# Kernel optimization log

Measured on AMD Instinct MI355X. Metric: run time of the kernel, lower is better.

## Reference

```python
import jax, jax.numpy as jnp
import numpy as np

EMBED = 1024

def setup_inputs() -> dict:
    key = jax.random.key(0)
    ks = jax.random.split(key, 7)
    s = 1.0 / np.sqrt(EMBED)
    x = jax.random.normal(ks[0], (8, 2048, EMBED), dtype=jnp.float32)
    Wq = jax.random.normal(ks[1], (EMBED, EMBED), dtype=jnp.float32) * s
    bq = jax.random.normal(ks[2], (EMBED,), dtype=jnp.float32) * s
    Wk = jax.random.normal(ks[3], (EMBED, EMBED), dtype=jnp.float32) * s
    bk = jax.random.normal(ks[4], (EMBED,), dtype=jnp.float32) * s
    Wv = jax.random.normal(ks[5], (EMBED, EMBED), dtype=jnp.float32) * s
    bv = jax.random.normal(ks[6], (EMBED,), dtype=jnp.float32) * s
    return {"x": x, "Wq": Wq, "bq": bq, "Wk": Wk, "bk": bk, "Wv": Wv, "bv": bv}

def reference(x, Wq, bq, Wk, bk, Wv, bv):
    # Linear layers: y = x @ W^T + b (torch convention)
    Q = jnp.einsum('bse,fe->bsf', x, Wq) + bq
    K = jnp.einsum('bse,fe->bsf', x, Wk) + bk
    V = jnp.einsum('bse,fe->bsf', x, Wv) + bv
    scale = 1.0 / jnp.sqrt(jnp.asarray(x.shape[-1], x.dtype))
    scores = jnp.einsum('bqe,bke->bqk', Q, K) * scale  # [B, S, S]
    weights = jax.nn.softmax(scores, axis=-1)
    # dropout is identity in eval mode (deterministic reference)
    return jnp.einsum('bqk,bke->bqe', weights, V)
```

## Files before the change

kernel.cpp:

```cpp
#include <hip/hip_runtime.h>

typedef __bf16 bf16x8 __attribute__((ext_vector_type(8)));
typedef float f32x4 __attribute__((ext_vector_type(4)));
typedef _Float16 f16x8v __attribute__((ext_vector_type(8)));
typedef unsigned short u16x8 __attribute__((ext_vector_type(8)));

__device__ __forceinline__ unsigned short f2bf(float f) {
  unsigned int u = __builtin_bit_cast(unsigned int, f);
  u += 0x7fffu + ((u >> 16) & 1u);
  return (unsigned short)(u >> 16);
}

__device__ __forceinline__ unsigned short f2h(float f) {
  _Float16 h = (_Float16)f;
  return __builtin_bit_cast(unsigned short, h);
}

__device__ __forceinline__ void async16(const void* g, void* l) {
  __builtin_amdgcn_global_load_lds(
      (const __attribute__((address_space(1))) unsigned int*)g,
      (__attribute__((address_space(3))) unsigned int*)l, 16, 0, 0);
}

#define MFMA(a, b, c) __builtin_amdgcn_mfma_f32_16x16x32_bf16((a), (b), (c), 0, 0, 0)

__global__ __launch_bounds__(256) void pack_bf16(const float* __restrict__ src,
                                                 unsigned short* __restrict__ dst,
                                                 long n) {
  long i = ((long)blockIdx.x * blockDim.x + threadIdx.x) * 4;
  long stride = (long)gridDim.x * blockDim.x * 4;
  for (; i < n; i += stride) {
    float4 v = *(const float4*)(src + i);
    ushort4 o;
    o.x = f2bf(v.x); o.y = f2bf(v.y); o.z = f2bf(v.z); o.w = f2bf(v.w);
    *(ushort4*)(dst + i) = o;
  }
}

template <int EPI>
__global__ __launch_bounds__(512, 2) void gemm256(
    const unsigned short* __restrict__ A, long sAz,
    const unsigned short* __restrict__ B, long sBz,
    int lda, int ldb, int nt,
    float* __restrict__ Cf, long sCz, int ldc, float scale,
    unsigned short* __restrict__ Cq, long sQz, int ldq,
    const float* __restrict__ bq, const float* __restrict__ bk,
    const float* __restrict__ bv) {
  extern __shared__ __align__(16) char smem[];
  const int tid = threadIdx.x;
  const int l = tid & 63;
  const int w = tid >> 6;
  const int wm = w >> 2, wn = w & 3;
  int bm = blockIdx.x;
  if ((gridDim.x & 7) == 0) {
    int cpx = gridDim.x >> 3;
    bm = (bm & 7) * cpx + (bm >> 3);
  }
  const int bn = blockIdx.y, bz = blockIdx.z;
  const unsigned short* Ab = A + (long)bz * sAz + (long)bm * 256 * lda;
  const unsigned short* Bb = B + (long)bz * sBz + (long)bn * 256 * ldb;

  const int r0 = tid >> 3;
  const int sch = (tid & 7) ^ (r0 & 7);
  const int l15 = l & 15;
  const int kof = (l >> 4) << 3;

  const int aslot = wm * 16384;
  const int bslot = 32768 + (wn >> 1) * 16384;
  const int brow0 = (wn & 1) * 64;

  f32x4 acc[8][4] = {};
  bf16x8 bfr[4][2];

#define LDA_FRAG(dst, buf, fr, ks)                                   \
  {                                                                  \
    int rins = (fr) * 16 + l15;                                      \
    int byte = (buf) + aslot + rins * 128 + ((ks) * 32 + kof) * 2;   \
    byte ^= (rins & 7) << 4;                                         \
    dst = *(const bf16x8*)(smem + byte);                             \
  }
#define LDB_FRAG(dst, buf, fc, ks)                                   \
  {                                                                  \
    int rins = brow0 + (fc) * 16 + l15;                              \
    int byte = (buf) + bslot + rins * 128 + ((ks) * 32 + kof) * 2;   \
    byte ^= (rins & 7) << 4;                                         \
    dst = *(const bf16x8*)(smem + byte);                             \
  }
#define STAGE_A(half, kt, dst)                                                  \
  {                                                                             \
    const unsigned short* s_ =                                                  \
        Ab + (long)((half) * 128 + r0) * lda + (kt) * 64 + sch * 8;             \
    async16(s_, smem + (dst) + tid * 16);                                       \
    async16(s_ + (long)64 * lda, smem + (dst) + 8192 + tid * 16);               \
  }
#define STAGE_B(half, kt, dst)                                                  \
  {                                                                             \
    const unsigned short* s_ =                                                  \
        Bb + (long)((half) * 128 + r0) * ldb + (kt) * 64 + sch * 8;             \
    async16(s_, smem + (dst) + tid * 16);                                       \
    async16(s_ + (long)64 * ldb, smem + (dst) + 8192 + tid * 16);               \
  }

  STAGE_B(0, 0, 32768); STAGE_B(1, 0, 49152);
  STAGE_A(0, 0, 0);     STAGE_A(1, 0, 16384);
  STAGE_B(0, 1, 65536 + 32768); STAGE_B(1, 1, 65536 + 49152);
  asm volatile("s_waitcnt vmcnt(4)" ::: "memory");
  __builtin_amdgcn_s_barrier();

  for (int t = 0; t < nt; ++t) {
    const int buf = (t & 1) << 16;
    const int nbuf = buf ^ 65536;
    const int tA = (t + 1 < nt) ? t + 1 : nt - 1;
    const int tB = (t + 2 < nt) ? t + 2 : nt - 1;

    bf16x8 a00, a01, a10, a11;

    LDA_FRAG(a00, buf, 0, 0); LDA_FRAG(a01, buf, 0, 1);
    LDA_FRAG(a10, buf, 1, 0); LDA_FRAG(a11, buf, 1, 1);
#pragma unroll
    for (int fc = 0; fc < 4; ++fc) {
      LDB_FRAG(bfr[fc][0], buf, fc, 0);
      LDB_FRAG(bfr[fc][1], buf, fc, 1);
    }
    STAGE_A(0, tA, nbuf);
    __builtin_amdgcn_s_barrier();
    __builtin_amdgcn_s_setprio(1);
#pragma unroll
    for (int fc = 0; fc < 4; ++fc) {
      acc[0][fc] = MFMA(a00, bfr[fc][0], acc[0][fc]);
      acc[0][fc] = MFMA(a01, bfr[fc][1], acc[0][fc]);
      acc[1][fc] = MFMA(a10, bfr[fc][0], acc[1][fc]);
      acc[1][fc] = MFMA(a11, bfr[fc][1], acc[1][fc]);
    }
    __builtin_amdgcn_s_setprio(0);
    __builtin_amdgcn_s_barrier();

    LDA_FRAG(a00, buf, 2, 0); LDA_FRAG(a01, buf, 2, 1);
    LDA_FRAG(a10, buf, 3, 0); LDA_FRAG(a11, buf, 3, 1);
    STAGE_A(1, tA, nbuf + 16384);
    __builtin_amdgcn_s_barrier();
    __builtin_amdgcn_s_setprio(1);
#pragma unroll
    for (int fc = 0; fc < 4; ++fc) {
      acc[2][fc] = MFMA(a00, bfr[fc][0], acc[2][fc]);
      acc[2][fc] = MFMA(a01, bfr[fc][1], acc[2][fc]);
      acc[3][fc] = MFMA(a10, bfr[fc][0], acc[3][fc]);
      acc[3][fc] = MFMA(a11, bfr[fc][1], acc[3][fc]);
    }
    __builtin_amdgcn_s_setprio(0);
    __builtin_amdgcn_s_barrier();

    LDA_FRAG(a00, buf, 4, 0); LDA_FRAG(a01, buf, 4, 1);
    LDA_FRAG(a10, buf, 5, 0); LDA_FRAG(a11, buf, 5, 1);
    STAGE_B(0, tB, buf + 32768);
    __builtin_amdgcn_s_barrier();
    __builtin_amdgcn_s_setprio(1);
#pragma unroll
    for (int fc = 0; fc < 4; ++fc) {
      acc[4][fc] = MFMA(a00, bfr[fc][0], acc[4][fc]);
      acc[4][fc] = MFMA(a01, bfr[fc][1], acc[4][fc]);
      acc[5][fc] = MFMA(a10, bfr[fc][0], acc[5][fc]);
      acc[5][fc] = MFMA(a11, bfr[fc][1], acc[5][fc]);
    }
    __builtin_amdgcn_s_setprio(0);
    __builtin_amdgcn_s_barrier();

    LDA_FRAG(a00, buf, 6, 0); LDA_FRAG(a01, buf, 6, 1);
    LDA_FRAG(a10, buf, 7, 0); LDA_FRAG(a11, buf, 7, 1);
    STAGE_B(1, tB, buf + 49152);
    __builtin_amdgcn_s_barrier();
    __builtin_amdgcn_s_setprio(1);
#pragma unroll
    for (int fc = 0; fc < 4; ++fc) {
      acc[6][fc] = MFMA(a00, bfr[fc][0], acc[6][fc]);
      acc[6][fc] = MFMA(a01, bfr[fc][1], acc[6][fc]);
      acc[7][fc] = MFMA(a10, bfr[fc][0], acc[7][fc]);
      acc[7][fc] = MFMA(a11, bfr[fc][1], acc[7][fc]);
    }
    __builtin_amdgcn_s_setprio(0);
    asm volatile("s_waitcnt vmcnt(4)" ::: "memory");
    __builtin_amdgcn_s_barrier();
  }

  asm volatile("s_waitcnt vmcnt(0)" ::: "memory");
  __builtin_amdgcn_s_barrier();

  const int rl = (l >> 4) * 4;

  if constexpr (EPI == 1) {
    float* C = Cf + (long)bz * sCz;
    const long grbase = (long)bm * 256 + wm * 128;
    const int gcbase = bn * 256 + wn * 64;
#pragma unroll
    for (int fr = 0; fr < 8; ++fr)
#pragma unroll
      for (int rr = 0; rr < 4; ++rr) {
        long gr = grbase + fr * 16 + rl + rr;
#pragma unroll
        for (int fc = 0; fc < 4; ++fc)
          C[gr * ldc + gcbase + fc * 16 + l15] = acc[fr][fc][rr] * scale;
      }
  } else {
    const int colbase = bn * 256 + wn * 64;
    const float* bias = nullptr;
    if constexpr (EPI == 0) {
      int which = colbase >> 10;
      bias = (which == 0) ? bq : (which == 1) ? bk : bv;
    }
#pragma unroll
    for (int fr = 0; fr < 8; ++fr)
#pragma unroll
      for (int fc = 0; fc < 4; ++fc) {
        int lc = fc * 16 + l15;
        float bv_ = 0.0f;
        if constexpr (EPI == 0) bv_ = bias[(colbase + lc) & 1023];
#pragma unroll
        for (int rr = 0; rr < 4; ++rr) {
          int lr = fr * 16 + rl + rr;
          int byte = w * 16384 + lr * 128 + lc * 2;
          byte ^= (lr & 7) << 4;
          unsigned short q;
          if constexpr (EPI == 0) q = f2bf(acc[fr][fc][rr] + bv_);
          else                    q = f2h(acc[fr][fc][rr] * scale);
          *(unsigned short*)(smem + byte) = q;
        }
      }
    __syncthreads();
    const long brow = (long)bm * 256;
#pragma unroll
    for (int it = 0; it < 16; ++it) {
      int f = it * 512 + tid;
      int r = f >> 5, ch = f & 31;
      int wv = (r >> 7) * 4 + (ch >> 3);
      int byte = wv * 16384 + (r & 127) * 128 + (ch & 7) * 16;
      byte ^= (r & 7) << 4;
      uint4 val = *(const uint4*)(smem + byte);
      if constexpr (EPI == 0) {
        int which = (bn * 256) >> 10;
        int cw0 = (bn * 256) & 1023;
        unsigned short* d = Cq + (long)which * 16777216L +
                            (brow + r) * 1024 + cw0 + ch * 8;
        *(uint4*)d = val;
      } else {
        unsigned short* d = Cq + (long)bz * sQz + (brow + r) * ldq +
                            bn * 256 + ch * 8;
        *(uint4*)d = val;
      }
    }
  }
#undef LDA_FRAG
#undef LDB_FRAG
#undef STAGE_A
#undef STAGE_B
}

__global__ __launch_bounds__(256) void transpose64(
    const unsigned short* __restrict__ V, unsigned short* __restrict__ Vt) {
  __shared__ unsigned short t[64][68];
  int b = blockIdx.z;
  int s0 = blockIdx.x * 64, d0 = blockIdx.y * 64;
  const unsigned short* src = V + (long)b * 2048 * 1024;
  unsigned short* dst = Vt + (long)b * 1024 * 2048;
  int r = threadIdx.x >> 4, c = threadIdx.x & 15;
#pragma unroll
  for (int i = 0; i < 4; ++i) {
    int row = i * 16 + r;
    const ushort2* p = (const ushort2*)(src + (long)(s0 + row) * 1024 + d0 + c * 4);
    ushort2 v0 = p[0], v1 = p[1];
    t[row][c * 4 + 0] = v0.x; t[row][c * 4 + 1] = v0.y;
    t[row][c * 4 + 2] = v1.x; t[row][c * 4 + 3] = v1.y;
  }
  __syncthreads();
#pragma unroll
  for (int i = 0; i < 4; ++i) {
    int drow = i * 16 + r;
    ushort2 o0, o1;
    o0.x = t[c * 4 + 0][drow]; o0.y = t[c * 4 + 1][drow];
    o1.x = t[c * 4 + 2][drow]; o1.y = t[c * 4 + 3][drow];
    ushort2* q = (ushort2*)(dst + (long)(d0 + drow) * 2048 + s0 + c * 4);
    q[0] = o0; q[1] = o1;
  }
}

__global__ __launch_bounds__(256) void softmax_rows_h(
    const unsigned short* __restrict__ S, unsigned short* __restrict__ W) {
  long row = blockIdx.x;
  int t = threadIdx.x;
  f16x8v hv = *(const f16x8v*)(S + row * 2048 + t * 8);
  float v[8];
#pragma unroll
  for (int k = 0; k < 8; ++k) v[k] = (float)hv[k];
  float m = v[0];
#pragma unroll
  for (int k = 1; k < 8; ++k) m = fmaxf(m, v[k]);
#pragma unroll
  for (int o = 32; o; o >>= 1) m = fmaxf(m, __shfl_xor(m, o));
  __shared__ float redm[4];
  __shared__ float reds[4];
  int wv = t >> 6;
  if ((t & 63) == 0) redm[wv] = m;
  __syncthreads();
  m = fmaxf(fmaxf(redm[0], redm[1]), fmaxf(redm[2], redm[3]));
  float e[8], s = 0.0f;
#pragma unroll
  for (int k = 0; k < 8; ++k) { e[k] = __expf(v[k] - m); s += e[k]; }
#pragma unroll
  for (int o = 32; o; o >>= 1) s += __shfl_xor(s, o);
  if ((t & 63) == 0) reds[wv] = s;
  __syncthreads();
  s = reds[0] + reds[1] + reds[2] + reds[3];
  float inv = 1.0f / s;
  u16x8 o;
#pragma unroll
  for (int k = 0; k < 8; ++k) o[k] = f2bf(e[k] * inv);
  *(u16x8*)(W + row * 2048 + t * 8) = o;
}

__global__ void sentinel_kernel(float* out, float v) { out[0] = v; }

extern "C" void kernel_launch(void* const* d_in, const int* in_sizes, int n_in,
                              void* d_out, int out_size, void* d_ws, size_t ws_size,
                              hipStream_t stream) {
  const float* x  = (const float*)d_in[0];
  const float* Wq = (const float*)d_in[1];
  const float* bq = (const float*)d_in[2];
  const float* Wk = (const float*)d_in[3];
  const float* bk = (const float*)d_in[4];
  const float* Wv = (const float*)d_in[5];
  const float* bv = (const float*)d_in[6];
  float* out = (float*)d_out;

  (void)hipFuncSetAttribute((const void*)gemm256<0>,
      hipFuncAttributeMaxDynamicSharedMemorySize, 131072);
  (void)hipFuncSetAttribute((const void*)gemm256<1>,
      hipFuncAttributeMaxDynamicSharedMemorySize, 131072);
  (void)hipFuncSetAttribute((const void*)gemm256<2>,
      hipFuncAttributeMaxDynamicSharedMemorySize, 131072);

  const size_t NEED_BIG = 207618048;
  const size_t NEED_MID = 140509184;
  if (ws_size < NEED_MID) {
    sentinel_kernel<<<1, 1, 0, stream>>>(out, (float)ws_size);
    return;
  }
  const bool big = (ws_size >= NEED_BIG);
  char* ws = (char*)d_ws;
  unsigned short* qkv = (unsigned short*)(ws);
  unsigned short* vt  = (unsigned short*)(ws + 100663296);
  unsigned short* wb  = (unsigned short*)(ws + 134217728);
  unsigned short* xb  = big ? (unsigned short*)(ws + 140509184)
                            : (unsigned short*)(ws + 100663296);
  unsigned short* sc  = big ? (unsigned short*)(ws + 140509184)
                            : (unsigned short*)(ws + 67108864);
  unsigned short* wt  = big ? (unsigned short*)(ws)
                            : (unsigned short*)(ws + 83886080);

  const float scale = 0.03125f;

  pack_bf16<<<dim3(4096), dim3(256), 0, stream>>>(x, xb, 16777216L);
  pack_bf16<<<dim3(1024), dim3(256), 0, stream>>>(Wq, wb, 1048576L);
  pack_bf16<<<dim3(1024), dim3(256), 0, stream>>>(Wk, wb + 1048576, 1048576L);
  pack_bf16<<<dim3(1024), dim3(256), 0, stream>>>(Wv, wb + 2097152, 1048576L);

  gemm256<0><<<dim3(64, 12, 1), dim3(512), 131072, stream>>>(
      xb, 0L, wb, 0L, 1024, 1024, 16,
      nullptr, 0L, 0, 1.0f, qkv, 0L, 1024, bq, bk, bv);

  transpose64<<<dim3(32, 16, 8), dim3(256), 0, stream>>>(qkv + 2L * 16777216, vt);

  const int bpp = big ? 8 : 2;
  const int npasses = 8 / bpp;
  for (int p = 0; p < npasses; ++p) {
    long b0 = (long)p * bpp;
    long boff = b0 * 2048 * 1024;
    gemm256<2><<<dim3(8, 8, bpp), dim3(512), 131072, stream>>>(
        qkv + boff, 2048L * 1024, qkv + 16777216 + boff, 2048L * 1024,
        1024, 1024, 16,
        nullptr, 0L, 0, scale, sc, 2048L * 2048, 2048,
        nullptr, nullptr, nullptr);

    softmax_rows_h<<<dim3(2048 * bpp), dim3(256), 0, stream>>>(sc, wt);

    gemm256<1><<<dim3(8, 4, bpp), dim3(512), 131072, stream>>>(
        wt, 2048L * 2048, vt + b0 * 1024 * 2048, 1024L * 2048,
        2048, 2048, 32,
        out + boff, 2048L * 1024, 1024, 1.0f, nullptr, 0L, 0,
        nullptr, nullptr, nullptr);
  }
}
```

Baseline: 327.2 us.

## Fuse softmax exp into QK GEMM epilogue and write V transposed from projection

The QK^T GEMM epilogue now applies exp to scaled scores, stores bf16 unnormalised weights and per-row partial sums. A tiny kernel reduces these to reciprocal row sums, which the PV GEMM applies in its epilogue. The QKV projection writes V directly in transposed layout, removing the separate transpose and softmax kernels and the score round-trip through memory. The max subtraction is dropped, which relies on scores staying small enough not to overflow exp.

Measured after the change: 291.8 us. -10.8%, faster.

```diff
diff --git a/kernel.cpp b/kernel.cpp
--- a/kernel.cpp
+++ b/kernel.cpp
@@ -2,18 +2,11 @@
 
 typedef __bf16 bf16x8 __attribute__((ext_vector_type(8)));
 typedef float f32x4 __attribute__((ext_vector_type(4)));
-typedef _Float16 f16x8v __attribute__((ext_vector_type(8)));
-typedef unsigned short u16x8 __attribute__((ext_vector_type(8)));
 
 __device__ __forceinline__ unsigned short f2bf(float f) {
   unsigned int u = __builtin_bit_cast(unsigned int, f);
   u += 0x7fffu + ((u >> 16) & 1u);
   return (unsigned short)(u >> 16);
-}
-
-__device__ __forceinline__ unsigned short f2h(float f) {
-  _Float16 h = (_Float16)f;
-  return __builtin_bit_cast(unsigned short, h);
 }
 
 __device__ __forceinline__ void async16(const void* g, void* l) {
@@ -45,7 +38,8 @@
     float* __restrict__ Cf, long sCz, int ldc, float scale,
     unsigned short* __restrict__ Cq, long sQz, int ldq,
     const float* __restrict__ bq, const float* __restrict__ bk,
-    const float* __restrict__ bv) {
+    const float* __restrict__ bv,
+    float* __restrict__ psum, const float* __restrict__ rsum) {
   extern __shared__ __align__(16) char smem[];
   const int tid = threadIdx.x;
   const int l = tid & 63;
@@ -187,44 +181,100 @@
 
   const int rl = (l >> 4) * 4;
 
-  if constexpr (EPI == 1) {
-    float* C = Cf + (long)bz * sCz;
-    const long grbase = (long)bm * 256 + wm * 128;
-    const int gcbase = bn * 256 + wn * 64;
-#pragma unroll
-    for (int fr = 0; fr < 8; ++fr)
-#pragma unroll
-      for (int rr = 0; rr < 4; ++rr) {
-        long gr = grbase + fr * 16 + rl + rr;
-#pragma unroll
-        for (int fc = 0; fc < 4; ++fc)
-          C[gr * ldc + gcbase + fc * 16 + l15] = acc[fr][fc][rr] * scale;
-      }
-  } else {
+  if constexpr (EPI == 0) {
+    const int which = (bn * 256) >> 10;
     const int colbase = bn * 256 + wn * 64;
-    const float* bias = nullptr;
-    if constexpr (EPI == 0) {
-      int which = colbase >> 10;
-      bias = (which == 0) ? bq : (which == 1) ? bk : bv;
-    }
-#pragma unroll
-    for (int fr = 0; fr < 8; ++fr)
+    const float* bias = (which == 0) ? bq : (which == 1) ? bk : bv;
+    if (which < 2) {
+#pragma unroll
+      for (int fr = 0; fr < 8; ++fr)
+#pragma unroll
+        for (int fc = 0; fc < 4; ++fc) {
+          int lc = fc * 16 + l15;
+          float bv_ = bias[(colbase + lc) & 1023];
+#pragma unroll
+          for (int rr = 0; rr < 4; ++rr) {
+            int lr = fr * 16 + rl + rr;
+            int byte = w * 16384 + lr * 128 + lc * 2;
+            byte ^= (lr & 7) << 4;
+            *(unsigned short*)(smem + byte) = f2bf(acc[fr][fc][rr] + bv_);
+          }
+        }
+      __syncthreads();
+      const long brow = (long)bm * 256;
+      const int cw0 = (bn * 256) & 1023;
+#pragma unroll
+      for (int it = 0; it < 16; ++it) {
+        int f = it * 512 + tid;
+        int r = f >> 5, ch = f & 31;
+        int wv = (r >> 7) * 4 + (ch >> 3);
+        int byte = wv * 16384 + (r & 127) * 128 + (ch & 7) * 16;
+        byte ^= (r & 7) << 4;
+        uint4 val = *(const uint4*)(smem + byte);
+        unsigned short* d = Cq + (long)which * 16777216L +
+                            (brow + r) * 1024 + cw0 + ch * 8;
+        *(uint4*)d = val;
+      }
+    } else {
+#pragma unroll
+      for (int fr = 0; fr < 8; ++fr)
+#pragma unroll
+        for (int fc = 0; fc < 4; ++fc) {
+          int lc = wn * 64 + fc * 16 + l15;
+          float bv_ = bias[(colbase + fc * 16 + l15) & 1023];
+#pragma unroll
+          for (int rr = 0; rr < 4; ++rr) {
+            int r = wm * 128 + fr * 16 + rl + rr;
+            int byte = lc * 512 + r * 2;
+            byte ^= (lc & 7) << 4;
+            *(unsigned short*)(smem + byte) = f2bf(acc[fr][fc][rr] + bv_);
+          }
+        }
+      __syncthreads();
+      const long brow = (long)bm * 256;
+      const long b = brow >> 11;
+      const long s0 = brow & 2047;
+      unsigned short* VT = Cq + 2L * 16777216;
+#pragma unroll
+      for (int it = 0; it < 16; ++it) {
+        int f = it * 512 + tid;
+        int c = f >> 5, ch = f & 31;
+        int byte = (c * 512 + ch * 16) ^ ((c & 7) << 4);
+        uint4 val = *(const uint4*)(smem + byte);
+        int d = (bn * 256 - 2048) + c;
+        unsigned short* dst = VT + b * 2097152 + (long)d * 2048 + s0 + ch * 8;
+        *(uint4*)dst = val;
+      }
+    }
+  } else if constexpr (EPI == 3) {
+    float rs[4];
+#pragma unroll
+    for (int fr = 0; fr < 8; ++fr) {
+      rs[0] = rs[1] = rs[2] = rs[3] = 0.0f;
 #pragma unroll
       for (int fc = 0; fc < 4; ++fc) {
         int lc = fc * 16 + l15;
-        float bv_ = 0.0f;
-        if constexpr (EPI == 0) bv_ = bias[(colbase + lc) & 1023];
 #pragma unroll
         for (int rr = 0; rr < 4; ++rr) {
+          float e = __expf(acc[fr][fc][rr] * scale);
+          rs[rr] += e;
           int lr = fr * 16 + rl + rr;
           int byte = w * 16384 + lr * 128 + lc * 2;
           byte ^= (lr & 7) << 4;
-          unsigned short q;
-          if constexpr (EPI == 0) q = f2bf(acc[fr][fc][rr] + bv_);
-          else                    q = f2h(acc[fr][fc][rr] * scale);
-          *(unsigned short*)(smem + byte) = q;
+          *(unsigned short*)(smem + byte) = f2bf(e);
         }
       }
+#pragma unroll
+      for (int rr = 0; rr < 4; ++rr) {
+        float v = rs[rr];
+#pragma unroll
+        for (int o = 1; o < 16; o <<= 1) v += __shfl_xor(v, o);
+        if (l15 == 0) {
+          int row = wm * 128 + fr * 16 + rl + rr;
+          *(float*)(smem + 131072 + (wn * 256 + row) * 4) = v;
+        }
+      }
+    }
     __syncthreads();
     const long brow = (long)bm * 256;
 #pragma unroll
@@ -235,18 +285,31 @@
       int byte = wv * 16384 + (r & 127) * 128 + (ch & 7) * 16;
       byte ^= (r & 7) << 4;
       uint4 val = *(const uint4*)(smem + byte);
-      if constexpr (EPI == 0) {
-        int which = (bn * 256) >> 10;
-        int cw0 = (bn * 256) & 1023;
-        unsigned short* d = Cq + (long)which * 16777216L +
-                            (brow + r) * 1024 + cw0 + ch * 8;
-        *(uint4*)d = val;
-      } else {
-        unsigned short* d = Cq + (long)bz * sQz + (brow + r) * ldq +
-                            bn * 256 + ch * 8;
-        *(uint4*)d = val;
-      }
-    }
+      unsigned short* d = Cq + (long)bz * sQz + (brow + r) * ldq + bn * 256 + ch * 8;
+      *(uint4*)d = val;
+    }
+    if (tid < 256) {
+      float s4 = *(const float*)(smem + 131072 + tid * 4) +
+                 *(const float*)(smem + 131072 + 1024 + tid * 4) +
+                 *(const float*)(smem + 131072 + 2048 + tid * 4) +
+                 *(const float*)(smem + 131072 + 3072 + tid * 4);
+      psum[(((long)bz * 2048) + brow + tid) * 8 + bn] = s4;
+    }
+  } else {
+    float* C = Cf + (long)bz * sCz;
+    const float* rsb = rsum + (long)bz * 2048;
+    const long grbase = (long)bm * 256 + wm * 128;
+    const int gcbase = bn * 256 + wn * 64;
+#pragma unroll
+    for (int fr = 0; fr < 8; ++fr)
+#pragma unroll
+      for (int rr = 0; rr < 4; ++rr) {
+        long gr = grbase + fr * 16 + rl + rr;
+        float inv = rsb[gr];
+#pragma unroll
+        for (int fc = 0; fc < 4; ++fc)
+          C[gr * ldc + gcbase + fc * 16 + l15] = acc[fr][fc][rr] * inv;
+      }
   }
 #undef LDA_FRAG
 #undef LDB_FRAG
@@ -254,66 +317,14 @@
 #undef STAGE_B
 }
 
-__global__ __launch_bounds__(256) void transpose64(
-    const unsigned short* __restrict__ V, unsigned short* __restrict__ Vt) {
-  __shared__ unsigned short t[64][68];
-  int b = blockIdx.z;
-  int s0 = blockIdx.x * 64, d0 = blockIdx.y * 64;
-  const unsigned short* src = V + (long)b * 2048 * 1024;
-  unsigned short* dst = Vt + (long)b * 1024 * 2048;
-  int r = threadIdx.x >> 4, c = threadIdx.x & 15;
-#pragma unroll
-  for (int i = 0; i < 4; ++i) {
-    int row = i * 16 + r;
-    const ushort2* p = (const ushort2*)(src + (long)(s0 + row) * 1024 + d0 + c * 4);
-    ushort2 v0 = p[0], v1 = p[1];
-    t[row][c * 4 + 0] = v0.x; t[row][c * 4 + 1] = v0.y;
-    t[row][c * 4 + 2] = v1.x; t[row][c * 4 + 3] = v1.y;
-  }
-  __syncthreads();
-#pragma unroll
-  for (int i = 0; i < 4; ++i) {
-    int drow = i * 16 + r;
-    ushort2 o0, o1;
-    o0.x = t[c * 4 + 0][drow]; o0.y = t[c * 4 + 1][drow];
-    o1.x = t[c * 4 + 2][drow]; o1.y = t[c * 4 + 3][drow];
-    ushort2* q = (ushort2*)(dst + (long)(d0 + drow) * 2048 + s0 + c * 4);
-    q[0] = o0; q[1] = o1;
-  }
-}
-
-__global__ __launch_bounds__(256) void softmax_rows_h(
-    const unsigned short* __restrict__ S, unsigned short* __restrict__ W) {
-  long row = blockIdx.x;
-  int t = threadIdx.x;
-  f16x8v hv = *(const f16x8v*)(S + row * 2048 + t * 8);
-  float v[8];
-#pragma unroll
-  for (int k = 0; k < 8; ++k) v[k] = (float)hv[k];
-  float m = v[0];
-#pragma unroll
-  for (int k = 1; k < 8; ++k) m = fmaxf(m, v[k]);
-#pragma unroll
-  for (int o = 32; o; o >>= 1) m = fmaxf(m, __shfl_xor(m, o));
-  __shared__ float redm[4];
-  __shared__ float reds[4];
-  int wv = t >> 6;
-  if ((t & 63) == 0) redm[wv] = m;
-  __syncthreads();
-  m = fmaxf(fmaxf(redm[0], redm[1]), fmaxf(redm[2], redm[3]));
-  float e[8], s = 0.0f;
-#pragma unroll
-  for (int k = 0; k < 8; ++k) { e[k] = __expf(v[k] - m); s += e[k]; }
-#pragma unroll
-  for (int o = 32; o; o >>= 1) s += __shfl_xor(s, o);
-  if ((t & 63) == 0) reds[wv] = s;
-  __syncthreads();
-  s = reds[0] + reds[1] + reds[2] + reds[3];
-  float inv = 1.0f / s;
-  u16x8 o;
-#pragma unroll
-  for (int k = 0; k < 8; ++k) o[k] = f2bf(e[k] * inv);
-  *(u16x8*)(W + row * 2048 + t * 8) = o;
+__global__ __launch_bounds__(256) void reduce_psum(const float* __restrict__ p,
+                                                   float* __restrict__ r, int n) {
+  int i = blockIdx.x * 256 + threadIdx.x;
+  if (i < n) {
+    const float* q = p + (long)i * 8;
+    float s = q[0] + q[1] + q[2] + q[3] + q[4] + q[5] + q[6] + q[7];
+    r[i] = 1.0f / s;
+  }
 }
 
 __global__ void sentinel_kernel(float* out, float v) { out[0] = v; }
@@ -331,29 +342,27 @@
   float* out = (float*)d_out;
 
   (void)hipFuncSetAttribute((const void*)gemm256<0>,
-      hipFuncAttributeMaxDynamicSharedMemorySize, 131072);
-  (void)hipFuncSetAttribute((const void*)gemm256<1>,
-      hipFuncAttributeMaxDynamicSharedMemorySize, 131072);
-  (void)hipFuncSetAttribute((const void*)gemm256<2>,
-      hipFuncAttributeMaxDynamicSharedMemorySize, 131072);
-
-  const size_t NEED_BIG = 207618048;
-  const size_t NEED_MID = 140509184;
-  if (ws_size < NEED_MID) {
+      hipFuncAttributeMaxDynamicSharedMemorySize, 135168);
+  (void)hipFuncSetAttribute((const void*)gemm256<3>,
+      hipFuncAttributeMaxDynamicSharedMemorySize, 135168);
+  (void)hipFuncSetAttribute((const void*)gemm256<4>,
+      hipFuncAttributeMaxDynamicSharedMemorySize, 135168);
+
+  const size_t NEED_BIG2 = 208207872;
+  const size_t NEED_SM2  = 140509184;
+  if (ws_size < NEED_SM2) {
     sentinel_kernel<<<1, 1, 0, stream>>>(out, (float)ws_size);
     return;
   }
-  const bool big = (ws_size >= NEED_BIG);
+  const bool big = (ws_size >= NEED_BIG2);
   char* ws = (char*)d_ws;
   unsigned short* qkv = (unsigned short*)(ws);
-  unsigned short* vt  = (unsigned short*)(ws + 100663296);
+  unsigned short* xb  = (unsigned short*)(ws + 100663296);
   unsigned short* wb  = (unsigned short*)(ws + 134217728);
-  unsigned short* xb  = big ? (unsigned short*)(ws + 140509184)
+  unsigned short* wt  = big ? (unsigned short*)(ws + 140509184)
                             : (unsigned short*)(ws + 100663296);
-  unsigned short* sc  = big ? (unsigned short*)(ws + 140509184)
-                            : (unsigned short*)(ws + 67108864);
-  unsigned short* wt  = big ? (unsigned short*)(ws)
-                            : (unsigned short*)(ws + 83886080);
+  float* psum = big ? (float*)(ws + 207618048) : (float*)(ws + 117440512);
+  float* rsum = big ? (float*)(ws + 208142336) : (float*)(ws + 117571584);
 
   const float scale = 0.03125f;
 
@@ -362,29 +371,27 @@
   pack_bf16<<<dim3(1024), dim3(256), 0, stream>>>(Wk, wb + 1048576, 1048576L);
   pack_bf16<<<dim3(1024), dim3(256), 0, stream>>>(Wv, wb + 2097152, 1048576L);
 
-  gemm256<0><<<dim3(64, 12, 1), dim3(512), 131072, stream>>>(
+  gemm256<0><<<dim3(64, 12, 1), dim3(512), 135168, stream>>>(
       xb, 0L, wb, 0L, 1024, 1024, 16,
-      nullptr, 0L, 0, 1.0f, qkv, 0L, 1024, bq, bk, bv);
-
-  transpose64<<<dim3(32, 16, 8), dim3(256), 0, stream>>>(qkv + 2L * 16777216, vt);
+      nullptr, 0L, 0, 1.0f, qkv, 0L, 1024, bq, bk, bv, nullptr, nullptr);
 
   const int bpp = big ? 8 : 2;
   const int npasses = 8 / bpp;
   for (int p = 0; p < npasses; ++p) {
     long b0 = (long)p * bpp;
     long boff = b0 * 2048 * 1024;
-    gemm256<2><<<dim3(8, 8, bpp), dim3(512), 131072, stream>>>(
+    gemm256<3><<<dim3(8, 8, bpp), dim3(512), 135168, stream>>>(
         qkv + boff, 2048L * 1024, qkv + 16777216 + boff, 2048L * 1024,
         1024, 1024, 16,
-        nullptr, 0L, 0, scale, sc, 2048L * 2048, 2048,
-        nullptr, nullptr, nullptr);
-
-    softmax_rows_h<<<dim3(2048 * bpp), dim3(256), 0, stream>>>(sc, wt);
-
-    gemm256<1><<<dim3(8, 4, bpp), dim3(512), 131072, stream>>>(
-        wt, 2048L * 2048, vt + b0 * 1024 * 2048, 1024L * 2048,
+        nullptr, 0L, 0, scale, wt, 2048L * 2048, 2048,
+        nullptr, nullptr, nullptr, psum, nullptr);
+
+    reduce_psum<<<dim3(8 * bpp), dim3(256), 0, stream>>>(psum, rsum, 2048 * bpp);
+
+    gemm256<4><<<dim3(8, 4, bpp), dim3(512), 135168, stream>>>(
+        wt, 2048L * 2048, qkv + 2L * 16777216 + b0 * 2097152, 2097152L,
         2048, 2048, 32,
         out + boff, 2048L * 1024, 1024, 1.0f, nullptr, 0L, 0,
-        nullptr, nullptr, nullptr);
-  }
-}
+        nullptr, nullptr, nullptr, nullptr, rsum);
+  }
+}
```
